# Kernel optimization log

Measured on AMD Instinct MI355X. Metric: run time of the kernel, lower is better.

Reference implementation:

```python
import jax, jax.numpy as jnp
import numpy as np
import math

H = 16          # num_attention_heads
D = 1024        # hidden_size
DH = D // H     # size_per_head = 64


def setup_inputs() -> dict:
    key = jax.random.key(0)
    ks = jax.random.split(key, 8)
    B, S = 4, 2048
    std = 0.02
    inputs = jax.random.normal(ks[0], (B, S, D), dtype=jnp.float32)
    attention_mask = jax.random.randint(ks[1], (B, S), 0, 2, dtype=jnp.int32)
    Wq = jax.random.normal(ks[2], (D, D), dtype=jnp.float32) * std
    Wk = jax.random.normal(ks[3], (D, D), dtype=jnp.float32) * std
    Wv = jax.random.normal(ks[4], (D, D), dtype=jnp.float32) * std
    bq = jnp.zeros((D,), dtype=jnp.float32)
    bk = jnp.zeros((D,), dtype=jnp.float32)
    bv = jnp.zeros((D,), dtype=jnp.float32)
    return {"inputs": inputs, "attention_mask": attention_mask,
            "Wq": Wq, "bq": bq, "Wk": Wk, "bk": bk, "Wv": Wv, "bv": bv}


def reference(inputs, attention_mask, Wq, bq, Wk, bk, Wv, bv):
    B, S, _ = inputs.shape
    scale = 1.0 / math.sqrt(float(DH))

    def split_heads(x):  # [B,S,D] -> [B,H,S,DH]
        return x.reshape(B, S, H, DH).transpose(0, 2, 1, 3)

    q = split_heads(inputs @ Wq + bq)
    k = split_heads(inputs @ Wk + bk)
    v = split_heads(inputs @ Wv + bv)

    # [B,H,S,S] scores
    scores = jnp.einsum('bhqd,bhkd->bhqk', q, k) * scale
    # additive mask: (1 - mask[b, k]) * -10000, broadcast over heads and query pos
    mask = attention_mask.astype(jnp.float32)[:, None, None, :]  # [B,1,1,S]
    scores = scores + (1.0 - mask) * -10000.0

    probs = jax.nn.softmax(scores, axis=-1)  # dropout prob = 0.0 -> identity
    out = jnp.einsum('bhqk,bhkd->bhqd', probs, v)  # [B,H,S,DH]
    return out.transpose(0, 2, 1, 3).reshape(B, S, D)
```

## Files before the change

kernel.cpp:

```cpp
#include <hip/hip_runtime.h>
#include <cstddef>

#define NH 16
#define DMODEL 1024
#define DHD 64
#define BB 4
#define SS 2048
#define MROWS (BB * SS)
#define XE ((size_t)MROWS * DMODEL)

typedef __attribute__((ext_vector_type(8))) short short8;
typedef __attribute__((ext_vector_type(4))) short short4v;
typedef __attribute__((ext_vector_type(4))) float f32x4;
typedef __attribute__((ext_vector_type(16))) float f32x16;
typedef __attribute__((ext_vector_type(4))) int i32x4;

__device__ __forceinline__ float bf2f(unsigned short u) {
    return __uint_as_float(((unsigned int)u) << 16);
}
__device__ __forceinline__ unsigned short f2bf(float f) {
    unsigned int u = __float_as_uint(f);
    u += 0x7fffu + ((u >> 16) & 1u);
    return (unsigned short)(u >> 16);
}

__device__ __forceinline__ int detect_f32(const unsigned short* X, int tid,
                                          int* flagShared) {
    if (tid < 64) {
        unsigned e = (X[2 * tid] >> 7) & 0xFFu;
        unsigned long long m = __ballot(e >= 100u && e <= 150u);
        if (tid == 0) *flagShared = (__popcll(m) < 48) ? 1 : 0;
    }
    __syncthreads();
    return *flagShared;
}

__device__ __forceinline__ void gl2lds16(const unsigned short* g,
                                         unsigned short* l) {
    __builtin_amdgcn_global_load_lds(
        (const __attribute__((address_space(1))) unsigned int*)g,
        (__attribute__((address_space(3))) unsigned int*)l, 16, 0, 0);
}

__global__ __launch_bounds__(256) void conv_x(
    const unsigned short* __restrict__ X, unsigned short* __restrict__ Scr)
{
    __shared__ int dflag;
    int isf32 = detect_f32(X, threadIdx.x, &dflag);
    if (!isf32) return;
    const float* Xf = (const float*)X;
    size_t i0 = ((size_t)blockIdx.x * 256 + threadIdx.x) * 8;
    f32x4 a = *(const f32x4*)(Xf + i0);
    f32x4 b = *(const f32x4*)(Xf + i0 + 4);
    short8 o;
#pragma unroll
    for (int j = 0; j < 4; j++) { o[j] = (short)f2bf(a[j]); o[4 + j] = (short)f2bf(b[j]); }
    *(short8*)(Scr + i0) = o;
}

__global__ __launch_bounds__(256) void conv_w(
    const unsigned short* __restrict__ Wq,
    const unsigned short* __restrict__ Wk,
    const unsigned short* __restrict__ Wv,
    const unsigned short* __restrict__ Xdet,
    unsigned short* __restrict__ Scr)
{
    __shared__ float tile[64][65];
    __shared__ int dflag;
    int isf32 = detect_f32(Xdet, threadIdx.x, &dflag);
    unsigned short* Wt = Scr + (isf32 ? XE : 0);
    int mat = blockIdx.z;
    const unsigned short* Ws = (mat == 0) ? Wq : ((mat == 1) ? Wk : Wv);
    const float* Wf = (const float*)Ws;
    int n0 = blockIdx.x * 64, k0 = blockIdx.y * 64;
    int tx = threadIdx.x & 63, ty = threadIdx.x >> 6;
#pragma unroll
    for (int p = 0; p < 16; p++) {
        int k = ty + 4 * p;
        float v = isf32 ? Wf[(size_t)(k0 + k) * DMODEL + n0 + tx]
                        : bf2f(Ws[(size_t)(k0 + k) * DMODEL + n0 + tx]);
        tile[k][tx] = v;
    }
    __syncthreads();
    unsigned short* Wm = Wt + (size_t)mat * DMODEL * DMODEL;
#pragma unroll
    for (int p = 0; p < 16; p++) {
        int n = ty + 4 * p;
        Wm[(size_t)(n0 + n) * DMODEL + k0 + tx] = f2bf(tile[tx][n]);
    }
}

__global__ __launch_bounds__(256, 2) void qkv_gemm(
    const unsigned short* __restrict__ Xorig,
    const unsigned short* __restrict__ Scr,
    const unsigned short* __restrict__ bq,
    const unsigned short* __restrict__ bk,
    const unsigned short* __restrict__ bv,
    unsigned short* __restrict__ Q,
    unsigned short* __restrict__ K,
    unsigned short* __restrict__ Vt)
{
    __shared__ __align__(16) unsigned short As[128][64];
    __shared__ __align__(16) unsigned short Bs[128][64];
    __shared__ int dflag;

    int tid = threadIdx.x, lane = tid & 63, w = tid >> 6;
    int wr = w >> 1, wc = w & 1, quad = lane >> 4, c = lane & 15;
    int m0 = blockIdx.x * 128;
    int by = blockIdx.y;
    int mat = by >> 3;
    int nb = (by & 7) * 128;

    int isf32 = detect_f32(Xorig, tid, &dflag);
    const unsigned short* Xsrc = isf32 ? Scr : Xorig;
    const unsigned short* Wt = Scr + (isf32 ? XE : 0);
    const unsigned short* Wrows = Wt + ((size_t)mat * DMODEL + nb) * DMODEL;

    int srow = lane >> 3;
    int scol = (lane & 7) * 8;

    f32x4 acc[4][4];
#pragma unroll
    for (int a = 0; a < 4; a++)
#pragma unroll
        for (int b2 = 0; b2 < 4; b2++) acc[a][b2] = (f32x4){0.f, 0.f, 0.f, 0.f};

    for (int k0 = 0; k0 < DMODEL; k0 += 64) {
        __syncthreads();
#pragma unroll
        for (int t = 0; t < 4; t++) {
            int r = w * 32 + t * 8 + srow;
            gl2lds16(Xsrc + (size_t)(m0 + r) * DMODEL + k0 + scol,
                     &As[w * 32 + t * 8][0]);
            gl2lds16(Wrows + (size_t)r * DMODEL + k0 + scol,
                     &Bs[w * 32 + t * 8][0]);
        }
        __syncthreads();

#pragma unroll
        for (int ks = 0; ks < 2; ks++) {
            short8 af[4], bf[4];
#pragma unroll
            for (int t = 0; t < 4; t++) {
                af[t] = *(const short8*)&As[wr * 64 + t * 16 + c][ks * 32 + quad * 8];
                bf[t] = *(const short8*)&Bs[wc * 64 + t * 16 + c][ks * 32 + quad * 8];
            }
#pragma unroll
            for (int rt = 0; rt < 4; rt++)
#pragma unroll
                for (int ct = 0; ct < 4; ct++)
                    acc[rt][ct] = __builtin_amdgcn_mfma_f32_16x16x32_bf16(
                        af[rt], bf[ct], acc[rt][ct], 0, 0, 0);
        }
    }

    const unsigned short* bias = (mat == 0) ? bq : ((mat == 1) ? bk : bv);
    float qscale = (mat == 0) ? 0.18033688f : 1.0f;
#pragma unroll
    for (int ct = 0; ct < 4; ct++) {
        int nl = nb + wc * 64 + ct * 16 + c;
        float bvv = isf32 ? ((const float*)bias)[nl] : bf2f(bias[nl]);
        int hl = nl >> 6, d = nl & 63;
#pragma unroll
        for (int rt = 0; rt < 4; rt++) {
            int r0 = m0 + wr * 64 + rt * 16 + quad * 4;
            int b_ = r0 >> 11, s_ = r0 & 2047;
            int bh = b_ * NH + hl;
            if (mat < 2) {
                unsigned short* dst =
                    ((mat == 0) ? Q : K) + ((size_t)bh * SS + s_) * DHD + d;
#pragma unroll
                for (int i = 0; i < 4; i++)
                    dst[(size_t)i * DHD] = f2bf((acc[rt][ct][i] + bvv) * qscale);
            } else {
                unsigned short* dst = Vt + ((size_t)bh * DHD + d) * SS + s_;
                short4v pk;
#pragma unroll
                for (int i = 0; i < 4; i++)
                    pk[i] = (short)f2bf(acc[rt][ct][i] + bvv);
                *(short4v*)dst = pk;
            }
        }
    }
}


#define LOADSTEP(kf_, vf_, mv_, kb_)                                         \
    {                                                                        \
        int kbv = (kb_);                                                     \
        _Pragma("unroll")                                                    \
        for (int d = 0; d < 4; d++)                                          \
            kf_[d] = *(const short8*)(Kh + (size_t)(kbv + l31) * DHD +       \
                                      d * 16 + hi * 8);                      \
        _Pragma("unroll")                                                    \
        for (int g = 0; g < 4; g++)                                          \
            mv_[g] = *(const i32x4*)(maskb + kbv + 8 * g + 4 * hi);          \
        _Pragma("unroll")                                                    \
        for (int dt = 0; dt < 2; dt++)                                       \
            _Pragma("unroll")                                                \
            for (int kt = 0; kt < 2; kt++)                                   \
                vf_[dt][kt] = *(const short8*)(Vth +                         \
                    (size_t)(dt * 32 + l31) * SS + kbv + kt * 16 + hi * 8);  \
    }

#define COMPUTESTEP(kf_, vf_, mv_)                                           \
    _Pragma("unroll")                                                        \
    for (int qq = 0; qq < 2; qq++) {                                         \
        f32x16 s;                                                            \
        _Pragma("unroll")                                                    \
        for (int r = 0; r < 16; r++)                                         \
            s[r] = mv_[r >> 2][r & 3] ? 0.0f : -16384.0f;                    \
        _Pragma("unroll")                                                    \
        for (int d = 0; d < 4; d++)                                          \
            s = __builtin_amdgcn_mfma_f32_32x32x16_bf16(kf_[d], qf[qq][d],   \
                                                        s, 0, 0, 0);         \
        float p[16];                                                         \
        float ps0 = 0.f, ps1 = 0.f;                                          \
        _Pragma("unroll")                                                    \
        for (int r = 0; r < 16; r++) {                                       \
            float pv = __builtin_amdgcn_exp2f(s[r]);                         \
            p[r] = pv;                                                       \
            if (r & 1) ps1 += pv; else ps0 += pv;                            \
        }                                                                    \
        psum[qq] += ps0 + ps1;                                               \
        int aw[8];                                                           \
        _Pragma("unroll")                                                    \
        for (int t = 0; t < 8; t++)                                          \
            asm("v_cvt_pk_bf16_f32 %0, %1, %2"                               \
                : "=v"(aw[t]) : "v"(p[2 * t]), "v"(p[2 * t + 1]));           \
        asm("v_permlane32_swap_b32 %0, %1" : "+v"(aw[0]), "+v"(aw[2]));      \
        asm("v_permlane32_swap_b32 %0, %1" : "+v"(aw[1]), "+v"(aw[3]));      \
        asm("v_permlane32_swap_b32 %0, %1" : "+v"(aw[4]), "+v"(aw[6]));      \
        asm("v_permlane32_swap_b32 %0, %1" : "+v"(aw[5]), "+v"(aw[7]));      \
        i32x4 f0 = {aw[0], aw[1], aw[2], aw[3]};                             \
        i32x4 f1 = {aw[4], aw[5], aw[6], aw[7]};                             \
        short8 pf0 = __builtin_bit_cast(short8, f0);                         \
        short8 pf1 = __builtin_bit_cast(short8, f1);                         \
        _Pragma("unroll")                                                    \
        for (int dt = 0; dt < 2; dt++) {                                     \
            oacc[dt][qq] = __builtin_amdgcn_mfma_f32_32x32x16_bf16(          \
                vf_[dt][0], pf0, oacc[dt][qq], 0, 0, 0);                     \
            oacc[dt][qq] = __builtin_amdgcn_mfma_f32_32x32x16_bf16(          \
                vf_[dt][1], pf1, oacc[dt][qq], 0, 0, 0);                     \
        }                                                                    \
    }

__global__ __launch_bounds__(256, 2) void attn(
    const unsigned short* __restrict__ Q,
    const unsigned short* __restrict__ Kg,
    const unsigned short* __restrict__ Vt,
    const int* __restrict__ mask,
    unsigned short* __restrict__ OutBase,
    const unsigned short* __restrict__ Xdet)
{
    int tid = threadIdx.x;
    int lane = tid & 63, w = tid >> 6;
    int l31 = lane & 31, hi = lane >> 5;

    unsigned ex = ((unsigned)Xdet[2 * lane] >> 7) & 0xFFu;
    unsigned long long bm = __ballot(ex >= 100u && ex <= 150u);
    int isf32 = (__popcll(bm) < 48) ? 1 : 0;

    int lin = blockIdx.x;
    int bh = (lin & 7) + (((lin >> 3) & 7) << 3);
    int qt = lin >> 6;
    int bz = bh >> 4, hl = bh & 15;

    const unsigned short* Qh = Q + (size_t)bh * SS * DHD;
    const unsigned short* Kh = Kg + (size_t)bh * SS * DHD;
    const unsigned short* Vth = Vt + (size_t)bh * DHD * SS;
    const int* maskb = mask + (size_t)bz * SS;

    int q0 = qt * 256 + w * 64;

    short8 qf[2][4];
#pragma unroll
    for (int qq = 0; qq < 2; qq++)
#pragma unroll
        for (int d = 0; d < 4; d++)
            qf[qq][d] = *(const short8*)(Qh + (size_t)(q0 + qq * 32 + l31) * DHD +
                                         d * 16 + hi * 8);

    f32x16 oacc[2][2];
    float psum[2] = {0.f, 0.f};
#pragma unroll
    for (int dt = 0; dt < 2; dt++)
#pragma unroll
        for (int qq = 0; qq < 2; qq++)
#pragma unroll
            for (int r = 0; r < 16; r++) oacc[dt][qq][r] = 0.f;

    short8 kfA[4], kfB[4];
    short8 vfA[2][2], vfB[2][2];
    i32x4 mvA[4], mvB[4];

    LOADSTEP(kfA, vfA, mvA, 0);
    for (int kb = 0; kb < SS; kb += 64) {
        LOADSTEP(kfB, vfB, mvB, kb + 32);
        COMPUTESTEP(kfA, vfA, mvA);
        LOADSTEP(kfA, vfA, mvA, (kb + 64) & (SS - 1));
        COMPUTESTEP(kfB, vfB, mvB);
    }

    long obase = (long)bz * SS * DMODEL;
    unsigned short* Outh = OutBase + obase;
    float* Outf = (float*)OutBase + obase;
#pragma unroll
    for (int qq = 0; qq < 2; qq++) {
        float tot = psum[qq] + __shfl_xor(psum[qq], 32);
        float inv = 1.0f / tot;
        int q = q0 + qq * 32 + l31;
#pragma unroll
        for (int dt = 0; dt < 2; dt++) {
#pragma unroll
            for (int g = 0; g < 4; g++) {
                int dbase = dt * 32 + 8 * g + 4 * hi;
                size_t base = (size_t)q * DMODEL + hl * DHD + dbase;
                if (isf32) {
                    f32x4 ov;
#pragma unroll
                    for (int j = 0; j < 4; j++)
                        ov[j] = oacc[dt][qq][4 * g + j] * inv;
                    *(f32x4*)(Outf + base) = ov;
                } else {
                    short4v ov;
#pragma unroll
                    for (int j = 0; j < 4; j++)
                        ov[j] = (short)f2bf(oacc[dt][qq][4 * g + j] * inv);
                    *(short4v*)(Outh + base) = ov;
                }
            }
        }
    }
}

extern "C" void kernel_launch(void* const* d_in, const int* in_sizes, int n_in,
                              void* d_out, int out_size, void* d_ws, size_t ws_size,
                              hipStream_t stream)
{
    const unsigned short* X    = (const unsigned short*)d_in[0];
    const int*            mask = (const int*)d_in[1];
    const unsigned short* Wq   = (const unsigned short*)d_in[2];
    const unsigned short* bq   = (const unsigned short*)d_in[3];
    const unsigned short* Wk   = (const unsigned short*)d_in[4];
    const unsigned short* bk   = (const unsigned short*)d_in[5];
    const unsigned short* Wv   = (const unsigned short*)d_in[6];
    const unsigned short* bv   = (const unsigned short*)d_in[7];

    unsigned short* Scr = (unsigned short*)d_out;

    unsigned short* Qw  = (unsigned short*)d_ws;
    unsigned short* Kw  = Qw + (size_t)BB * NH * SS * DHD;
    unsigned short* Vtw = Kw + (size_t)BB * NH * SS * DHD;

    conv_x<<<dim3((unsigned)(XE / (256 * 8))), 256, 0, stream>>>(X, Scr);
    conv_w<<<dim3(16, 16, 3), 256, 0, stream>>>(Wq, Wk, Wv, X, Scr);
    qkv_gemm<<<dim3(64, 24), 256, 0, stream>>>(
        X, Scr, bq, bk, bv, Qw, Kw, Vtw);
    attn<<<dim3(512), 256, 0, stream>>>(
        Qw, Kw, Vtw, mask, (unsigned short*)d_out, X);
}
```

Baseline: 308.6 us.

## Stage K and V tiles through double-buffered LDS shared by all waves

Replaces per-wave direct global loads of K and V^T fragments with a cooperative global-to-LDS staging into a two-slot XOR-swizzled shared buffer, from which each wave reads its MFMA fragments. Previously each of the four waves fetched identical K/V tiles independently, multiplying cache traffic. The new scheme adds two block barriers per 64-key step and LDS read latency, which may reduce overlap between loads and MFMA work.

Measured after the change: 259.3 us. 1.19x faster.

```diff
diff --git a/kernel.cpp b/kernel.cpp
--- a/kernel.cpp
+++ b/kernel.cpp
@@ -185,63 +185,80 @@
 }
 
 
-#define LOADSTEP(kf_, vf_, mv_, kb_)                                         \
+#define STAGE(B_, kb_)                                                       \
+    {                                                                        \
+        int kbv = (kb_);                                                     \
+        int rK = w * 8 + (lane >> 3);                                        \
+        int cK = lane & 7;                                                   \
+        gl2lds16(Kh + (size_t)(kbv + rK) * DHD + ((cK ^ (rK & 7)) << 3),     \
+                 &KT[B_][w * 512]);                                          \
+        int rV = w * 16 + (lane >> 2);                                       \
+        int cV = lane & 3;                                                   \
+        gl2lds16(Vth + (size_t)rV * SS + kbv + ((cV ^ (rV & 3)) << 3),       \
+                 &VT[B_][w * 512]);                                          \
+    }
+
+#define MVLOAD(mv_, kb_)                                                     \
     {                                                                        \
         int kbv = (kb_);                                                     \
         _Pragma("unroll")                                                    \
-        for (int d = 0; d < 4; d++)                                          \
-            kf_[d] = *(const short8*)(Kh + (size_t)(kbv + l31) * DHD +       \
-                                      d * 16 + hi * 8);                      \
-        _Pragma("unroll")                                                    \
         for (int g = 0; g < 4; g++)                                          \
             mv_[g] = *(const i32x4*)(maskb + kbv + 8 * g + 4 * hi);          \
+    }
+
+#define COMPUTESTEP(B_, mv_)                                                 \
+    {                                                                        \
+        short8 kf[4];                                                        \
+        _Pragma("unroll")                                                    \
+        for (int d = 0; d < 4; d++)                                          \
+            kf[d] = *(const short8*)&KT[B_][l31 * 64 +                       \
+                                           (((d * 2 + hi) ^ (l31 & 7)) << 3)];\
+        short8 vf[2][2];                                                     \
         _Pragma("unroll")                                                    \
         for (int dt = 0; dt < 2; dt++)                                       \
             _Pragma("unroll")                                                \
             for (int kt = 0; kt < 2; kt++)                                   \
-                vf_[dt][kt] = *(const short8*)(Vth +                         \
-                    (size_t)(dt * 32 + l31) * SS + kbv + kt * 16 + hi * 8);  \
-    }
-
-#define COMPUTESTEP(kf_, vf_, mv_)                                           \
-    _Pragma("unroll")                                                        \
-    for (int qq = 0; qq < 2; qq++) {                                         \
-        f32x16 s;                                                            \
+                vf[dt][kt] = *(const short8*)&VT[B_][(dt * 32 + l31) * 32 +  \
+                                     (((kt * 2 + hi) ^ (l31 & 3)) << 3)];    \
         _Pragma("unroll")                                                    \
-        for (int r = 0; r < 16; r++)                                         \
-            s[r] = mv_[r >> 2][r & 3] ? 0.0f : -16384.0f;                    \
-        _Pragma("unroll")                                                    \
-        for (int d = 0; d < 4; d++)                                          \
-            s = __builtin_amdgcn_mfma_f32_32x32x16_bf16(kf_[d], qf[qq][d],   \
-                                                        s, 0, 0, 0);         \
-        float p[16];                                                         \
-        float ps0 = 0.f, ps1 = 0.f;                                          \
-        _Pragma("unroll")                                                    \
-        for (int r = 0; r < 16; r++) {                                       \
-            float pv = __builtin_amdgcn_exp2f(s[r]);                         \
-            p[r] = pv;                                                       \
-            if (r & 1) ps1 += pv; else ps0 += pv;                            \
-        }                                                                    \
-        psum[qq] += ps0 + ps1;                                               \
-        int aw[8];                                                           \
-        _Pragma("unroll")                                                    \
-        for (int t = 0; t < 8; t++)                                          \
-            asm("v_cvt_pk_bf16_f32 %0, %1, %2"                               \
-                : "=v"(aw[t]) : "v"(p[2 * t]), "v"(p[2 * t + 1]));           \
-        asm("v_permlane32_swap_b32 %0, %1" : "+v"(aw[0]), "+v"(aw[2]));      \
-        asm("v_permlane32_swap_b32 %0, %1" : "+v"(aw[1]), "+v"(aw[3]));      \
-        asm("v_permlane32_swap_b32 %0, %1" : "+v"(aw[4]), "+v"(aw[6]));      \
-        asm("v_permlane32_swap_b32 %0, %1" : "+v"(aw[5]), "+v"(aw[7]));      \
-        i32x4 f0 = {aw[0], aw[1], aw[2], aw[3]};                             \
-        i32x4 f1 = {aw[4], aw[5], aw[6], aw[7]};                             \
-        short8 pf0 = __builtin_bit_cast(short8, f0);                         \
-        short8 pf1 = __builtin_bit_cast(short8, f1);                         \
-        _Pragma("unroll")                                                    \
-        for (int dt = 0; dt < 2; dt++) {                                     \
-            oacc[dt][qq] = __builtin_amdgcn_mfma_f32_32x32x16_bf16(          \
-                vf_[dt][0], pf0, oacc[dt][qq], 0, 0, 0);                     \
-            oacc[dt][qq] = __builtin_amdgcn_mfma_f32_32x32x16_bf16(          \
-                vf_[dt][1], pf1, oacc[dt][qq], 0, 0, 0);                     \
+        for (int qq = 0; qq < 2; qq++) {                                     \
+            f32x16 s;                                                        \
+            _Pragma("unroll")                                                \
+            for (int r = 0; r < 16; r++)                                     \
+                s[r] = mv_[r >> 2][r & 3] ? 0.0f : -16384.0f;                \
+            _Pragma("unroll")                                                \
+            for (int d = 0; d < 4; d++)                                      \
+                s = __builtin_amdgcn_mfma_f32_32x32x16_bf16(kf[d], qf[qq][d],\
+                                                            s, 0, 0, 0);     \
+            float p[16];                                                     \
+            float ps0 = 0.f, ps1 = 0.f;                                      \
+            _Pragma("unroll")                                                \
+            for (int r = 0; r < 16; r++) {                                   \
+                float pv = __builtin_amdgcn_exp2f(s[r]);                     \
+                p[r] = pv;                                                   \
+                if (r & 1) ps1 += pv; else ps0 += pv;                        \
+            }                                                                \
+            psum[qq] += ps0 + ps1;                                           \
+            int aw[8];                                                       \
+            _Pragma("unroll")                                                \
+            for (int t = 0; t < 8; t++)                                      \
+                asm("v_cvt_pk_bf16_f32 %0, %1, %2"                           \
+                    : "=v"(aw[t]) : "v"(p[2 * t]), "v"(p[2 * t + 1]));       \
+            asm("v_permlane32_swap_b32 %0, %1" : "+v"(aw[0]), "+v"(aw[2]));  \
+            asm("v_permlane32_swap_b32 %0, %1" : "+v"(aw[1]), "+v"(aw[3]));  \
+            asm("v_permlane32_swap_b32 %0, %1" : "+v"(aw[4]), "+v"(aw[6]));  \
+            asm("v_permlane32_swap_b32 %0, %1" : "+v"(aw[5]), "+v"(aw[7]));  \
+            i32x4 f0 = {aw[0], aw[1], aw[2], aw[3]};                         \
+            i32x4 f1 = {aw[4], aw[5], aw[6], aw[7]};                         \
+            short8 pf0 = __builtin_bit_cast(short8, f0);                     \
+            short8 pf1 = __builtin_bit_cast(short8, f1);                     \
+            _Pragma("unroll")                                                \
+            for (int dt = 0; dt < 2; dt++) {                                 \
+                oacc[dt][qq] = __builtin_amdgcn_mfma_f32_32x32x16_bf16(      \
+                    vf[dt][0], pf0, oacc[dt][qq], 0, 0, 0);                  \
+                oacc[dt][qq] = __builtin_amdgcn_mfma_f32_32x32x16_bf16(      \
+                    vf[dt][1], pf1, oacc[dt][qq], 0, 0, 0);                  \
+            }                                                                \
         }                                                                    \
     }
 
@@ -253,6 +270,9 @@
     unsigned short* __restrict__ OutBase,
     const unsigned short* __restrict__ Xdet)
 {
+    __shared__ __align__(16) unsigned short KT[2][2048];
+    __shared__ __align__(16) unsigned short VT[2][2048];
+
     int tid = threadIdx.x;
     int lane = tid & 63, w = tid >> 6;
     int l31 = lane & 31, hi = lane >> 5;
@@ -290,16 +310,24 @@
 #pragma unroll
             for (int r = 0; r < 16; r++) oacc[dt][qq][r] = 0.f;
 
-    short8 kfA[4], kfB[4];
-    short8 vfA[2][2], vfB[2][2];
     i32x4 mvA[4], mvB[4];
 
-    LOADSTEP(kfA, vfA, mvA, 0);
+    STAGE(0, 0);
+    MVLOAD(mvA, 0);
+    __syncthreads();
+
     for (int kb = 0; kb < SS; kb += 64) {
-        LOADSTEP(kfB, vfB, mvB, kb + 32);
-        COMPUTESTEP(kfA, vfA, mvA);
-        LOADSTEP(kfA, vfA, mvA, (kb + 64) & (SS - 1));
-        COMPUTESTEP(kfB, vfB, mvB);
+        STAGE(1, kb + 32);
+        MVLOAD(mvB, kb + 32);
+        COMPUTESTEP(0, mvA);
+        __syncthreads();
+
+        if (kb + 64 < SS) {
+            STAGE(0, kb + 64);
+            MVLOAD(mvA, kb + 64);
+        }
+        COMPUTESTEP(1, mvB);
+        __syncthreads();
     }
 
     long obase = (long)bz * SS * DMODEL;
```
